# Performance work log

Measured on AMD Instinct MI355X. Metric: run time of the kernel, lower is better.

The kernel has to match this reference:

```python
import jax, jax.numpy as jnp
from jax import lax
import numpy as np

P = 9  # patch_size


def unfold9(img):
    # img: (C, H, W) -> (C, P*P, L) with L = (H//P)*(W//P), non-overlapping patches
    C, H, W = img.shape
    x = img.reshape(C, H // P, P, W // P, P)
    x = x.transpose(0, 2, 4, 1, 3).reshape(C, P * P, (H // P) * (W // P))
    return x


def fold9(blocks, H, W):
    # blocks: (C, P*P, L) -> (C, H, W), inverse of unfold9 (no overlaps)
    C = blocks.shape[0]
    x = blocks.reshape(C, P, P, H // P, W // P)
    return x.transpose(0, 3, 1, 4, 2).reshape(C, H, W)


def avgpool3d_k3s2p1(x):
    # AvgPool3d(kernel=3, stride=2, padding=1, count_include_pad=False) on (B,C,D,H,W)
    win = (1, 1, 3, 3, 3)
    strides = (1, 1, 2, 2, 2)
    pad = [(0, 0), (0, 0), (1, 1), (1, 1), (1, 1)]
    s = lax.reduce_window(x, 0.0, lax.add, win, strides, pad)
    cnt = lax.reduce_window(jnp.ones_like(x[:1, :1]), 0.0, lax.add, win, strides, pad)
    return s / cnt


def setup_inputs() -> dict:
    key = jax.random.key(0)
    k = jax.random.split(key, 7)
    in1, in2, out = 32, 64, 64
    x = jax.random.normal(k[0], (1, in1, 36, 72, 72), jnp.float32)
    y = jax.random.normal(k[1], (1, in2, 18, 36, 36), jnp.float32)
    z = jax.random.normal(k[2], (1, out, 36, 72, 72), jnp.float32)
    w_img = jax.random.normal(k[3], (out, in1), jnp.float32) * 0.05
    b_img = jax.random.normal(k[4], (out,), jnp.float32) * 0.01
    w_fea = jax.random.normal(k[5], (out, in2), jnp.float32) * 0.05
    b_fea = jax.random.normal(k[6], (out,), jnp.float32) * 0.01
    return {"x": x, "y": y, "z": z, "w_img": w_img, "b_img": b_img,
            "w_fea": w_fea, "b_fea": b_fea}


def reference(x, y, z, w_img, b_img, w_fea, b_fea):
    # 1x1x1 conv projections (pointwise channel mix)
    xq = jnp.einsum('bcdhw,oc->bodhw', x, w_img) + b_img[None, :, None, None, None]
    yk = jnp.einsum('bcdhw,oc->bodhw', y, w_fea) + b_fea[None, :, None, None, None]
    C = xq.shape[1]
    D1, HW1 = xq.shape[2], xq.shape[3] * xq.shape[4]
    D2, HW2 = yk.shape[2], yk.shape[3] * yk.shape[4]
    Ux = unfold9(xq.reshape(C, D1, HW1))          # (C, 81, L1)
    Uy = unfold9(yk.reshape(C, D2, HW2))          # (C, 81, L2)
    att = jnp.einsum('ckl,ckm->clm', Ux, Uy)      # (C, L1, L2) per-channel patch attn

    # --- Cross_head ---
    Dd, Hd, Wd = z.shape[2], z.shape[3], z.shape[4]
    dec = z.reshape(C, Dd, Hd * Wd)               # decoder_reshape
    xd = avgpool3d_k3s2p1(z)                      # (1, C, Dd', Hd', Wd')
    Dp, HWp = xd.shape[2], xd.shape[3] * xd.shape[4]
    Uxd = unfold9(xd.reshape(C, Dp, HWp))         # (C, 81, L2)
    # count_nonzero along L2 (non-differentiable, matches torch)
    nz = jnp.sum(att != 0, axis=-1).astype(att.dtype) + 1e-5  # (C, L1)
    corr_blocks = jnp.einsum('clm,ckm->ckl', att / nz[:, :, None], Uxd)  # (C, 81, L1)
    corr = fold9(corr_blocks, Dd, Hd * Wd)        # (C, Dd, Hd*Wd)
    act = jnp.where(corr > 0, corr, 0.2 * corr)   # LeakyReLU(0.2)
    out = act * dec + dec
    return out.reshape(z.shape)
```

## Files before the change

### kernel.cpp

```cpp
#include <hip/hip_runtime.h>
#include <hip/hip_bf16.h>

typedef __hip_bfloat16 bf16;
typedef float in_t;
typedef float out_t;
typedef __attribute__((ext_vector_type(8))) short short8;
typedef __attribute__((ext_vector_type(4))) float f32x4;

#define CH    64
#define CIN1  32
#define CIN2  64
#define S1    186624
#define W1    5184
#define S2    23328
#define W2    1296
#define LDSTR 1297
#define BSTR  104
#define XSTR  134
#define OSTR  136
#define YSTR  68
#define HWSTR 76
#define INV_NZ (1.0f/(288.0f + 1e-5f))

#define NB_PL 1152
#define NB_PX 1458
#define NB_PY 365

static __device__ __forceinline__ unsigned short f2bu(float f) {
    bf16 h = __float2bfloat16(f);
    unsigned short u;
    __builtin_memcpy(&u, &h, 2);
    return u;
}

__global__ __launch_bounds__(256) void k_stage1(
    const in_t* __restrict__ x, const in_t* __restrict__ wi, const in_t* __restrict__ bi,
    bf16* __restrict__ xq,
    const in_t* __restrict__ y, const in_t* __restrict__ wf, const in_t* __restrict__ bf,
    float* __restrict__ yk,
    const in_t* __restrict__ z, float* __restrict__ xd)
{
    __shared__ __align__(16) char smem[22528];
    int bid = blockIdx.x;
    int t   = threadIdx.x;

    if (bid < NB_PL) {
        float* dsum = reinterpret_cast<float*>(smem);
        int c = bid / 18, od = bid - (bid/18)*18;
        int dlo = od ? 2*od - 1 : 0;
        int nd  = od ? 3 : 2;
        const float4* zp = reinterpret_cast<const float4*>(z + ((size_t)c*36 + dlo)*W1);
        if (nd == 3) {
            for (int i = t; i < 1296; i += 256) {
                float4 a = zp[i], b = zp[1296 + i], e = zp[2592 + i];
                float4 s = { a.x+b.x+e.x, a.y+b.y+e.y, a.z+b.z+e.z, a.w+b.w+e.w };
                int r = i / 18, q = i - (i/18)*18;
                *reinterpret_cast<float4*>(&dsum[r*HWSTR + q*4]) = s;
            }
        } else {
            for (int i = t; i < 1296; i += 256) {
                float4 a = zp[i], b = zp[1296 + i];
                float4 s = { a.x+b.x, a.y+b.y, a.z+b.z, a.w+b.w };
                int r = i / 18, q = i - (i/18)*18;
                *reinterpret_cast<float4*>(&dsum[r*HWSTR + q*4]) = s;
            }
        }
        __syncthreads();
        float icd = (nd == 3) ? (1.f/3.f) : 0.5f;
        float* xdp = xd + (size_t)c*S2 + (size_t)od*W2;
        for (int idx = t; idx < 1296; idx += 256) {
            int oh = idx / 36, ow = idx - (idx/36)*36;
            int h0 = oh ? 2*oh-1 : 0, h1 = 2*oh+1;
            int w0 = ow ? 2*ow-1 : 0, w1 = 2*ow+1;
            float s = 0.f;
            for (int h = h0; h <= h1; ++h)
                for (int w = w0; w <= w1; ++w)
                    s += dsum[h*HWSTR + w];
            float ich = (h1 - h0) == 1 ? 0.5f : (1.f/3.f);
            float icw = (w1 - w0) == 1 ? 0.5f : (1.f/3.f);
            xdp[idx] = s * icd * ich * icw;
        }
    } else if (bid < NB_PL + NB_PX) {
        float*          xl = reinterpret_cast<float*>(smem);
        unsigned short* wl = reinterpret_cast<unsigned short*>(smem + CIN1*XSTR*4);
        int gs0 = (bid - NB_PL)*128;
        #pragma unroll
        for (int i = 0; i < 4; ++i) {
            int fi = t + i*256;
            int c  = fi >> 5, s4 = fi & 31;
            float4 v = *reinterpret_cast<const float4*>(&x[(size_t)c*S1 + gs0 + s4*4]);
            float* dst = &xl[c*XSTR + s4*4];
            *reinterpret_cast<float2*>(dst)     = (float2){v.x, v.y};
            *reinterpret_cast<float2*>(dst + 2) = (float2){v.z, v.w};
        }
        #pragma unroll
        for (int i = 0; i < 2; ++i) {
            int wj = t + i*256;
            int o  = wj >> 3, c4 = wj & 7;
            float4 v = *reinterpret_cast<const float4*>(&wi[o*CIN1 + c4*4]);
            ushort4 u = { f2bu(v.x), f2bu(v.y), f2bu(v.z), f2bu(v.w) };
            *reinterpret_cast<ushort4*>(&wl[o*CIN1 + c4*4]) = u;
        }
        int l = t & 63, wv = t >> 6;
        int lcol = l & 15, loct = l >> 4;
        float bly[4];
        #pragma unroll
        for (int og = 0; og < 4; ++og) bly[og] = bi[og*16 + lcol];
        __syncthreads();

        short8 wfr[4];
        #pragma unroll
        for (int og = 0; og < 4; ++og)
            wfr[og] = *reinterpret_cast<const short8*>(&wl[(og*16 + lcol)*CIN1 + loct*8]);

        ushort4 rr[2][4];
        #pragma unroll
        for (int mt = 0; mt < 2; ++mt) {
            int s_base = (wv*2 + mt)*16;
            union { short8 v; unsigned short u[8]; } af;
            #pragma unroll
            for (int j = 0; j < 8; ++j)
                af.u[j] = f2bu(xl[(loct*8 + j)*XSTR + s_base + lcol]);
            #pragma unroll
            for (int og = 0; og < 4; ++og) {
                f32x4 d = { bly[og], bly[og], bly[og], bly[og] };
                d = __builtin_amdgcn_mfma_f32_16x16x32_bf16(af.v, wfr[og], d, 0, 0, 0);
                rr[mt][og] = (ushort4){ f2bu(d[0]), f2bu(d[1]), f2bu(d[2]), f2bu(d[3]) };
            }
        }
        __syncthreads();
        unsigned short* ot = reinterpret_cast<unsigned short*>(smem);
        #pragma unroll
        for (int mt = 0; mt < 2; ++mt)
            #pragma unroll
            for (int og = 0; og < 4; ++og)
                *reinterpret_cast<ushort4*>(
                    &ot[(og*16 + lcol)*OSTR + wv*32 + mt*16 + loct*4]) = rr[mt][og];
        __syncthreads();
        #pragma unroll
        for (int j = 0; j < 4; ++j) {
            int row = wv*16 + j*4 + (l >> 4);
            int c8  = l & 15;
            uint4 v = *reinterpret_cast<const uint4*>(&ot[row*OSTR + c8*8]);
            *reinterpret_cast<uint4*>(
                (unsigned short*)xq + (size_t)row*S1 + gs0 + c8*8) = v;
        }
    } else {
        int pyb   = bid - NB_PL - NB_PX;
        int sblk0 = pyb*64;
        int wv = t >> 6, l = t & 63;
        int lcol = l & 15, loct = l >> 4;
        int tile = pyb*4 + wv;
        float* ot = reinterpret_cast<float*>(smem);
        bool act = (tile < 1458);
        f32x4 dv[4];
        if (act) {
            int s0 = tile*16;
            union { short8 v; unsigned short u[8]; } af[2];
            #pragma unroll
            for (int kk = 0; kk < 2; ++kk)
                #pragma unroll
                for (int j = 0; j < 8; ++j)
                    af[kk].u[j] = f2bu(y[(size_t)(kk*32 + loct*8 + j)*S2 + s0 + lcol]);
            #pragma unroll
            for (int og = 0; og < 4; ++og) {
                int o = og*16 + lcol;
                union { short8 v; unsigned short u[8]; } wfr[2];
                #pragma unroll
                for (int kk = 0; kk < 2; ++kk) {
                    float4 a  = *reinterpret_cast<const float4*>(&wf[o*CIN2 + kk*32 + loct*8]);
                    float4 bq = *reinterpret_cast<const float4*>(&wf[o*CIN2 + kk*32 + loct*8 + 4]);
                    wfr[kk].u[0]=f2bu(a.x);  wfr[kk].u[1]=f2bu(a.y);
                    wfr[kk].u[2]=f2bu(a.z);  wfr[kk].u[3]=f2bu(a.w);
                    wfr[kk].u[4]=f2bu(bq.x); wfr[kk].u[5]=f2bu(bq.y);
                    wfr[kk].u[6]=f2bu(bq.z); wfr[kk].u[7]=f2bu(bq.w);
                }
                float bo = bf[o];
                f32x4 d = { bo, bo, bo, bo };
                d = __builtin_amdgcn_mfma_f32_16x16x32_bf16(af[0].v, wfr[0].v, d, 0, 0, 0);
                d = __builtin_amdgcn_mfma_f32_16x16x32_bf16(af[1].v, wfr[1].v, d, 0, 0, 0);
                dv[og] = d;
            }
            #pragma unroll
            for (int og = 0; og < 4; ++og)
                *reinterpret_cast<float4*>(
                    &ot[(og*16 + lcol)*YSTR + wv*16 + loct*4]) =
                    (float4){ dv[og][0], dv[og][1], dv[og][2], dv[og][3] };
        }
        __syncthreads();
        #pragma unroll
        for (int j = 0; j < 4; ++j) {
            int row = wv*16 + j*4 + (l >> 4);
            int c4  = l & 15;
            int s   = sblk0 + c4*4;
            if (s < S2) {
                float4 v = *reinterpret_cast<const float4*>(&ot[row*YSTR + c4*4]);
                *reinterpret_cast<float4*>(&yk[(size_t)row*S2 + s]) = v;
            }
        }
    }
}

__global__ __launch_bounds__(256) void k_M(
    const float* __restrict__ xd, const float* __restrict__ yk, unsigned short* __restrict__ Mg)
{
    __shared__ float xl[3*LDSTR];
    __shared__ float yl[3*LDSTR];
    int b = blockIdx.x;
    int c = b / 9, r = b - c*9;
    int g = r / 3, h = r - g*3;
    int t = threadIdx.x;
    int t1 = t / 27, t2 = t - (t/27)*27;
    int offx[3];
    #pragma unroll
    for (int a = 0; a < 3; ++a) {
        int kl = t1*3 + a;
        offx[a] = (kl/9)*LDSTR + (kl - (kl/9)*9);
    }
    int offy = (t2/9)*LDSTR + (t2 - (t2/9)*9);
    float acc[3] = {};
    for (int ph2 = 0; ph2 < 2; ++ph2) {
        __syncthreads();
        for (int idx = t; idx < 3*W2; idx += 256) {
            int rr = idx / W2, col = idx - rr*W2;
            xl[rr*LDSTR + col] = xd[c*S2 + (ph2*9 + g*3 + rr)*W2 + col];
            yl[rr*LDSTR + col] = yk[c*S2 + (ph2*9 + h*3 + rr)*W2 + col];
        }
        __syncthreads();
        if (t < 243) {
            for (int m = 0; m < 144; ++m) {
                int cb = m*9;
                float yv = yl[cb + offy];
                #pragma unroll
                for (int a = 0; a < 3; ++a)
                    acc[a] += xl[cb + offx[a]] * yv;
            }
        }
    }
    if (t < 243) {
        #pragma unroll
        for (int a = 0; a < 3; ++a) {
            int k1 = g*27 + t1*3 + a;
            Mg[c*9216 + k1*96 + (h*27 + t2)] = f2bu(acc[a]);
        }
    }
    if (r == 0) {
        for (int idx = t; idx < 2655; idx += 256) {
            int row, col;
            if (idx < 1440) { int q = idx/96; row = 81 + q; col = idx - q*96; }
            else { int j = idx - 1440; int q = j/15; row = q; col = 81 + (j - q*15); }
            Mg[c*9216 + row*96 + col] = 0;
        }
    }
}

__global__ __launch_bounds__(256, 4) void k_corr(
    const unsigned short* __restrict__ Mg, const bf16* __restrict__ xq,
    const in_t* __restrict__ z, out_t* __restrict__ out)
{
    __shared__ __align__(16) unsigned short Pl[192*BSTR];
    int bid = blockIdx.x;
    int c   = bid / 12;
    int rem = bid - c*12;
    int ph  = rem / 3;
    int ck  = rem - ph*3;
    int colbase = ck*1728;
    int t = threadIdx.x;

    for (int idx = t; idx < 192*15; idx += 256) {
        int r = idx/15;
        Pl[r*BSTR + 81 + (idx - r*15)] = 0;
    }
    const unsigned short* xqu =
        (const unsigned short*)(xq + (size_t)c*S1 + (size_t)(ph*9)*W1 + colbase);
    for (int idx = t; idx < 3888; idx += 256) {
        int i2 = idx / 432, v4 = idx - i2*432;
        ushort4 vv = *reinterpret_cast<const ushort4*>(xqu + (size_t)i2*W1 + v4*4);
        int col = v4*4;
        unsigned short uu[4] = {vv.x, vv.y, vv.z, vv.w};
        #pragma unroll
        for (int j = 0; j < 4; ++j) {
            int cc = col + j;
            int p = cc/9, j2 = cc - p*9;
            Pl[p*BSTR + i2*9 + j2] = uu[j];
        }
    }
    __syncthreads();

    int wv = t >> 6, l = t & 63;
    int lrow = l & 15, lhi = l >> 4;

    short8 bfr[3][3];
    #pragma unroll
    for (int ntl = 0; ntl < 3; ++ntl) {
        int n = (wv*3 + ntl)*16 + lrow;
        #pragma unroll
        for (int kk = 0; kk < 3; ++kk)
            bfr[ntl][kk] = *reinterpret_cast<const short8*>(&Pl[n*BSTR + kk*32 + lhi*8]);
    }

    f32x4 acc[6][3];
    #pragma unroll
    for (int mt = 0; mt < 6; ++mt)
        #pragma unroll
        for (int ntl = 0; ntl < 3; ++ntl)
            acc[mt][ntl] = (f32x4){0.f,0.f,0.f,0.f};

    const unsigned short* Mc = Mg + c*9216;
    #pragma unroll
    for (int mt = 0; mt < 6; ++mt) {
        short8 afr[3];
        #pragma unroll
        for (int kk = 0; kk < 3; ++kk)
            afr[kk] = *reinterpret_cast<const short8*>(Mc + (mt*16 + lrow)*96 + kk*32 + lhi*8);
        #pragma unroll
        for (int ntl = 0; ntl < 3; ++ntl) {
            f32x4 d = acc[mt][ntl];
            #pragma unroll
            for (int kk = 0; kk < 3; ++kk)
                d = __builtin_amdgcn_mfma_f32_16x16x32_bf16(afr[kk], bfr[ntl][kk], d, 0, 0, 0);
            acc[mt][ntl] = d;
        }
    }
    __syncthreads();

    float* stage = reinterpret_cast<float*>(Pl);
    #pragma unroll
    for (int pass = 0; pass < 2; ++pass) {
        if ((wv >> 1) == pass) {
            #pragma unroll
            for (int mt = 0; mt < 6; ++mt)
                #pragma unroll
                for (int ntl = 0; ntl < 3; ++ntl) {
                    int n = (wv*3 + ntl)*16 + lrow - pass*96;
                    #pragma unroll
                    for (int r = 0; r < 4; ++r) {
                        int m = mt*16 + lhi*4 + r;
                        if (m <= 80) {
                            int i = m/9, j = m - 9*i;
                            stage[i*864 + n*9 + j] = acc[mt][ntl][r];
                        }
                    }
                }
        }
        __syncthreads();
        for (int idx = t; idx < 1944; idx += 256) {
            int i = idx/216, c4 = idx - i*216;
            float4 sv = *reinterpret_cast<const float4*>(&stage[i*864 + c4*4]);
            int ga = c*S1 + (ph*9 + i)*W1 + colbase + pass*864 + c4*4;
            float4 dv = *reinterpret_cast<const float4*>(&z[ga]);
            float4 ov;
            float cr;
            cr = sv.x*INV_NZ; ov.x = dv.x + (cr > 0.f ? cr : 0.2f*cr)*dv.x;
            cr = sv.y*INV_NZ; ov.y = dv.y + (cr > 0.f ? cr : 0.2f*cr)*dv.y;
            cr = sv.z*INV_NZ; ov.z = dv.z + (cr > 0.f ? cr : 0.2f*cr)*dv.z;
            cr = sv.w*INV_NZ; ov.w = dv.w + (cr > 0.f ? cr : 0.2f*cr)*dv.w;
            *reinterpret_cast<float4*>(&out[ga]) = ov;
        }
        __syncthreads();
    }
}

extern "C" void kernel_launch(void* const* d_in, const int* in_sizes, int n_in,
                              void* d_out, int out_size, void* d_ws, size_t ws_size,
                              hipStream_t stream)
{
    (void)in_sizes; (void)n_in; (void)out_size; (void)ws_size;
    const in_t* x     = (const in_t*)d_in[0];
    const in_t* y     = (const in_t*)d_in[1];
    const in_t* z     = (const in_t*)d_in[2];
    const in_t* w_img = (const in_t*)d_in[3];
    const in_t* b_img = (const in_t*)d_in[4];
    const in_t* w_fea = (const in_t*)d_in[5];
    const in_t* b_fea = (const in_t*)d_in[6];
    out_t* out = (out_t*)d_out;

    char* ws = (char*)d_ws;
    bf16*           xq = (bf16*)          (ws + 0);
    float*          yk = (float*)         (ws + 23887872);
    float*          xd = (float*)         (ws + 29859840);
    unsigned short* Mg = (unsigned short*)(ws + 35831808);

    hipLaunchKernelGGL(k_stage1, dim3(NB_PL + NB_PX + NB_PY), dim3(256), 0, stream,
                       x, w_img, b_img, xq, y, w_fea, b_fea, yk, z, xd);
    hipLaunchKernelGGL(k_M,      dim3(576), dim3(256), 0, stream, xd, yk, Mg);
    hipLaunchKernelGGL(k_corr,   dim3(768), dim3(256), 0, stream, Mg, xq, z, out);
}
```

Measured before the change: 82.08 us.

## Fuse three stage kernels into one persistent cooperative kernel with grid syncs

Merges the projection/pooling, M-computation and correlation kernels into a single cooperative launch. Each block loops over the virtual block indices of each stage, and grid-wide barriers separate the stages. This is meant to remove two kernel launch boundaries and their drain/ramp gaps. In exchange, shared memory is sized for the largest stage, the grid is capped by occupancy, grid.sync adds its own cost, and the launch-bounds hint now applies to all stages.

```diff
diff --git a/kernel.cpp b/kernel.cpp
--- a/kernel.cpp
+++ b/kernel.cpp
@@ -1,5 +1,8 @@
 #include <hip/hip_runtime.h>
 #include <hip/hip_bf16.h>
+#include <hip/hip_cooperative_groups.h>
+
+namespace cg = cooperative_groups;
 
 typedef __hip_bfloat16 bf16;
 typedef float in_t;
@@ -25,6 +28,9 @@
 #define NB_PL 1152
 #define NB_PX 1458
 #define NB_PY 365
+#define NBA   (NB_PL + NB_PX + NB_PY)
+#define NBB   576
+#define NBC   768
 
 static __device__ __forceinline__ unsigned short f2bu(float f) {
     bf16 h = __float2bfloat16(f);
@@ -33,20 +39,16 @@
     return u;
 }
 
-__global__ __launch_bounds__(256) void k_stage1(
+static __device__ void stageA_body(int vb, int t, char* smem,
     const in_t* __restrict__ x, const in_t* __restrict__ wi, const in_t* __restrict__ bi,
     bf16* __restrict__ xq,
-    const in_t* __restrict__ y, const in_t* __restrict__ wf, const in_t* __restrict__ bf,
+    const in_t* __restrict__ y, const in_t* __restrict__ wfe, const in_t* __restrict__ bfe,
     float* __restrict__ yk,
     const in_t* __restrict__ z, float* __restrict__ xd)
 {
-    __shared__ __align__(16) char smem[22528];
-    int bid = blockIdx.x;
-    int t   = threadIdx.x;
-
-    if (bid < NB_PL) {
+    if (vb < NB_PL) {
         float* dsum = reinterpret_cast<float*>(smem);
-        int c = bid / 18, od = bid - (bid/18)*18;
+        int c = vb / 18, od = vb - (vb/18)*18;
         int dlo = od ? 2*od - 1 : 0;
         int nd  = od ? 3 : 2;
         const float4* zp = reinterpret_cast<const float4*>(z + ((size_t)c*36 + dlo)*W1);
@@ -80,10 +82,10 @@
             float icw = (w1 - w0) == 1 ? 0.5f : (1.f/3.f);
             xdp[idx] = s * icd * ich * icw;
         }
-    } else if (bid < NB_PL + NB_PX) {
+    } else if (vb < NB_PL + NB_PX) {
         float*          xl = reinterpret_cast<float*>(smem);
         unsigned short* wl = reinterpret_cast<unsigned short*>(smem + CIN1*XSTR*4);
-        int gs0 = (bid - NB_PL)*128;
+        int gs0 = (vb - NB_PL)*128;
         #pragma unroll
         for (int i = 0; i < 4; ++i) {
             int fi = t + i*256;
@@ -146,15 +148,13 @@
                 (unsigned short*)xq + (size_t)row*S1 + gs0 + c8*8) = v;
         }
     } else {
-        int pyb   = bid - NB_PL - NB_PX;
+        int pyb   = vb - NB_PL - NB_PX;
         int sblk0 = pyb*64;
         int wv = t >> 6, l = t & 63;
         int lcol = l & 15, loct = l >> 4;
         int tile = pyb*4 + wv;
         float* ot = reinterpret_cast<float*>(smem);
-        bool act = (tile < 1458);
-        f32x4 dv[4];
-        if (act) {
+        if (tile < 1458) {
             int s0 = tile*16;
             union { short8 v; unsigned short u[8]; } af[2];
             #pragma unroll
@@ -168,24 +168,21 @@
                 union { short8 v; unsigned short u[8]; } wfr[2];
                 #pragma unroll
                 for (int kk = 0; kk < 2; ++kk) {
-                    float4 a  = *reinterpret_cast<const float4*>(&wf[o*CIN2 + kk*32 + loct*8]);
-                    float4 bq = *reinterpret_cast<const float4*>(&wf[o*CIN2 + kk*32 + loct*8 + 4]);
+                    float4 a  = *reinterpret_cast<const float4*>(&wfe[o*CIN2 + kk*32 + loct*8]);
+                    float4 bq = *reinterpret_cast<const float4*>(&wfe[o*CIN2 + kk*32 + loct*8 + 4]);
                     wfr[kk].u[0]=f2bu(a.x);  wfr[kk].u[1]=f2bu(a.y);
                     wfr[kk].u[2]=f2bu(a.z);  wfr[kk].u[3]=f2bu(a.w);
                     wfr[kk].u[4]=f2bu(bq.x); wfr[kk].u[5]=f2bu(bq.y);
                     wfr[kk].u[6]=f2bu(bq.z); wfr[kk].u[7]=f2bu(bq.w);
                 }
-                float bo = bf[o];
+                float bo = bfe[o];
                 f32x4 d = { bo, bo, bo, bo };
                 d = __builtin_amdgcn_mfma_f32_16x16x32_bf16(af[0].v, wfr[0].v, d, 0, 0, 0);
                 d = __builtin_amdgcn_mfma_f32_16x16x32_bf16(af[1].v, wfr[1].v, d, 0, 0, 0);
-                dv[og] = d;
-            }
-            #pragma unroll
-            for (int og = 0; og < 4; ++og)
                 *reinterpret_cast<float4*>(
                     &ot[(og*16 + lcol)*YSTR + wv*16 + loct*4]) =
-                    (float4){ dv[og][0], dv[og][1], dv[og][2], dv[og][3] };
+                    (float4){ d[0], d[1], d[2], d[3] };
+            }
         }
         __syncthreads();
         #pragma unroll
@@ -201,15 +198,14 @@
     }
 }
 
-__global__ __launch_bounds__(256) void k_M(
-    const float* __restrict__ xd, const float* __restrict__ yk, unsigned short* __restrict__ Mg)
+static __device__ void kM_body(int vb, int t, char* smem,
+    const float* __restrict__ xd, const float* __restrict__ yk,
+    unsigned short* __restrict__ Mg)
 {
-    __shared__ float xl[3*LDSTR];
-    __shared__ float yl[3*LDSTR];
-    int b = blockIdx.x;
-    int c = b / 9, r = b - c*9;
+    float* xl = reinterpret_cast<float*>(smem);
+    float* yl = xl + 3*LDSTR;
+    int c = vb / 9, r = vb - c*9;
     int g = r / 3, h = r - g*3;
-    int t = threadIdx.x;
     int t1 = t / 27, t2 = t - (t/27)*27;
     int offx[3];
     #pragma unroll
@@ -254,18 +250,16 @@
     }
 }
 
-__global__ __launch_bounds__(256, 4) void k_corr(
+static __device__ void kcorr_body(int vb, int t, char* smem,
     const unsigned short* __restrict__ Mg, const bf16* __restrict__ xq,
     const in_t* __restrict__ z, out_t* __restrict__ out)
 {
-    __shared__ __align__(16) unsigned short Pl[192*BSTR];
-    int bid = blockIdx.x;
-    int c   = bid / 12;
-    int rem = bid - c*12;
+    unsigned short* Pl = reinterpret_cast<unsigned short*>(smem);
+    int c   = vb / 12;
+    int rem = vb - c*12;
     int ph  = rem / 3;
     int ck  = rem - ph*3;
     int colbase = ck*1728;
-    int t = threadIdx.x;
 
     for (int idx = t; idx < 192*15; idx += 256) {
         int r = idx/15;
@@ -324,7 +318,7 @@
     }
     __syncthreads();
 
-    float* stage = reinterpret_cast<float*>(Pl);
+    float* stage = reinterpret_cast<float*>(smem);
     #pragma unroll
     for (int pass = 0; pass < 2; ++pass) {
         if ((wv >> 1) == pass) {
@@ -361,6 +355,34 @@
     }
 }
 
+__global__ __launch_bounds__(256, 4) void k_fused(
+    const in_t* __restrict__ x, const in_t* __restrict__ wi, const in_t* __restrict__ bi,
+    bf16* __restrict__ xq,
+    const in_t* __restrict__ y, const in_t* __restrict__ wfe, const in_t* __restrict__ bfe,
+    float* __restrict__ yk,
+    const in_t* __restrict__ z, float* __restrict__ xd,
+    unsigned short* __restrict__ Mg, out_t* __restrict__ out)
+{
+    __shared__ __align__(16) char smem[40960];
+    cg::grid_group grid = cg::this_grid();
+    int t = threadIdx.x;
+
+    for (int vb = blockIdx.x; vb < NBA; vb += gridDim.x) {
+        __syncthreads();
+        stageA_body(vb, t, smem, x, wi, bi, xq, y, wfe, bfe, yk, z, xd);
+    }
+    grid.sync();
+    for (int vb = blockIdx.x; vb < NBB; vb += gridDim.x) {
+        __syncthreads();
+        kM_body(vb, t, smem, xd, yk, Mg);
+    }
+    grid.sync();
+    for (int vb = blockIdx.x; vb < NBC; vb += gridDim.x) {
+        __syncthreads();
+        kcorr_body(vb, t, smem, Mg, xq, z, out);
+    }
+}
+
 extern "C" void kernel_launch(void* const* d_in, const int* in_sizes, int n_in,
                               void* d_out, int out_size, void* d_ws, size_t ws_size,
                               hipStream_t stream)
@@ -381,8 +403,16 @@
     float*          xd = (float*)         (ws + 29859840);
     unsigned short* Mg = (unsigned short*)(ws + 35831808);
 
-    hipLaunchKernelGGL(k_stage1, dim3(NB_PL + NB_PX + NB_PY), dim3(256), 0, stream,
-                       x, w_img, b_img, xq, y, w_fea, b_fea, yk, z, xd);
-    hipLaunchKernelGGL(k_M,      dim3(576), dim3(256), 0, stream, xd, yk, Mg);
-    hipLaunchKernelGGL(k_corr,   dim3(768), dim3(256), 0, stream, Mg, xq, z, out);
-}
+    int nb = 0;
+    if (hipOccupancyMaxActiveBlocksPerMultiprocessor(&nb, (const void*)k_fused, 256, 0)
+            != hipSuccess || nb < 1)
+        nb = 1;
+    int grid = nb * 256;
+    if (grid > 1024) grid = 1024;
+
+    void* args[] = { (void*)&x, (void*)&w_img, (void*)&b_img, (void*)&xq,
+                     (void*)&y, (void*)&w_fea, (void*)&b_fea, (void*)&yk,
+                     (void*)&z, (void*)&xd, (void*)&Mg, (void*)&out };
+    hipLaunchCooperativeKernel((const void*)k_fused, dim3(grid), dim3(256),
+                               args, 0, stream);
+}
```

Measured after the change: 302.2 us. 268% more time.

## Store pooled and projected intermediates as bf16 and split pooling blocks by half-height

Applied to the files above, without the earlier changes.

The intermediates yk (projected features) and xd (pooled decoder) are now written as bf16 instead of fp32 and expanded back to float when k_M loads them, halving their global traffic. The pooling blocks are also split into two halves along output height, doubling the pooling block count so each block reads and reduces fewer rows. This adds bf16 rounding ahead of the attention-matrix reduction, which may change accuracy, and the split reloads one overlapping input row per half.

```diff
diff --git a/kernel.cpp b/kernel.cpp
--- a/kernel.cpp
+++ b/kernel.cpp
@@ -22,7 +22,7 @@
 #define HWSTR 76
 #define INV_NZ (1.0f/(288.0f + 1e-5f))
 
-#define NB_PL 1152
+#define NB_PL 2304
 #define NB_PX 1458
 #define NB_PY 365
 
@@ -32,53 +32,66 @@
     __builtin_memcpy(&u, &h, 2);
     return u;
 }
+static __device__ __forceinline__ float bu2f(unsigned short u) {
+    unsigned int v = ((unsigned int)u) << 16;
+    float f;
+    __builtin_memcpy(&f, &v, 4);
+    return f;
+}
 
 __global__ __launch_bounds__(256) void k_stage1(
     const in_t* __restrict__ x, const in_t* __restrict__ wi, const in_t* __restrict__ bi,
     bf16* __restrict__ xq,
     const in_t* __restrict__ y, const in_t* __restrict__ wf, const in_t* __restrict__ bf,
-    float* __restrict__ yk,
-    const in_t* __restrict__ z, float* __restrict__ xd)
+    unsigned short* __restrict__ yk,
+    const in_t* __restrict__ z, unsigned short* __restrict__ xd)
 {
-    __shared__ __align__(16) char smem[22528];
+    __shared__ __align__(16) char smem[21504];
     int bid = blockIdx.x;
     int t   = threadIdx.x;
 
     if (bid < NB_PL) {
         float* dsum = reinterpret_cast<float*>(smem);
-        int c = bid / 18, od = bid - (bid/18)*18;
+        int c  = bid / 36;
+        int rr = bid - c*36;
+        int od = rr >> 1, half = rr & 1;
+        int hbase = half ? 35 : 0;
+        int nrows = half ? 37 : 36;
+        int oh0   = half ? 18 : 0;
         int dlo = od ? 2*od - 1 : 0;
         int nd  = od ? 3 : 2;
-        const float4* zp = reinterpret_cast<const float4*>(z + ((size_t)c*36 + dlo)*W1);
-        if (nd == 3) {
-            for (int i = t; i < 1296; i += 256) {
-                float4 a = zp[i], b = zp[1296 + i], e = zp[2592 + i];
-                float4 s = { a.x+b.x+e.x, a.y+b.y+e.y, a.z+b.z+e.z, a.w+b.w+e.w };
-                int r = i / 18, q = i - (i/18)*18;
-                *reinterpret_cast<float4*>(&dsum[r*HWSTR + q*4]) = s;
-            }
-        } else {
-            for (int i = t; i < 1296; i += 256) {
-                float4 a = zp[i], b = zp[1296 + i];
-                float4 s = { a.x+b.x, a.y+b.y, a.z+b.z, a.w+b.w };
-                int r = i / 18, q = i - (i/18)*18;
-                *reinterpret_cast<float4*>(&dsum[r*HWSTR + q*4]) = s;
-            }
+        const float* zb = z + ((size_t)c*36 + dlo)*W1;
+        for (int i = t; i < nrows*18; i += 256) {
+            int r = i / 18, q = i - (i/18)*18;
+            int off = (hbase + r)*18 + q;
+            const float4* p0 = reinterpret_cast<const float4*>(zb);
+            float4 a = p0[off], b = p0[1296 + off];
+            float4 s;
+            if (nd == 3) {
+                float4 e = p0[2592 + off];
+                s = (float4){ a.x+b.x+e.x, a.y+b.y+e.y, a.z+b.z+e.z, a.w+b.w+e.w };
+            } else {
+                s = (float4){ a.x+b.x, a.y+b.y, a.z+b.z, a.w+b.w };
+            }
+            *reinterpret_cast<float4*>(&dsum[r*HWSTR + q*4]) = s;
         }
         __syncthreads();
         float icd = (nd == 3) ? (1.f/3.f) : 0.5f;
-        float* xdp = xd + (size_t)c*S2 + (size_t)od*W2;
-        for (int idx = t; idx < 1296; idx += 256) {
-            int oh = idx / 36, ow = idx - (idx/36)*36;
+        unsigned short* xdp = xd + (size_t)c*S2 + (size_t)od*W2 + oh0*36;
+        for (int idx = t; idx < 648; idx += 256) {
+            int ohl = idx / 36, ow = idx - (idx/36)*36;
+            int oh = oh0 + ohl;
             int h0 = oh ? 2*oh-1 : 0, h1 = 2*oh+1;
             int w0 = ow ? 2*ow-1 : 0, w1 = 2*ow+1;
             float s = 0.f;
-            for (int h = h0; h <= h1; ++h)
+            for (int h = h0; h <= h1; ++h) {
+                int lr = h - hbase;
                 for (int w = w0; w <= w1; ++w)
-                    s += dsum[h*HWSTR + w];
+                    s += dsum[lr*HWSTR + w];
+            }
             float ich = (h1 - h0) == 1 ? 0.5f : (1.f/3.f);
             float icw = (w1 - w0) == 1 ? 0.5f : (1.f/3.f);
-            xdp[idx] = s * icd * ich * icw;
+            xdp[idx] = f2bu(s * icd * ich * icw);
         }
     } else if (bid < NB_PL + NB_PX) {
         float*          xl = reinterpret_cast<float*>(smem);
@@ -151,10 +164,8 @@
         int wv = t >> 6, l = t & 63;
         int lcol = l & 15, loct = l >> 4;
         int tile = pyb*4 + wv;
-        float* ot = reinterpret_cast<float*>(smem);
-        bool act = (tile < 1458);
-        f32x4 dv[4];
-        if (act) {
+        unsigned short* ot = reinterpret_cast<unsigned short*>(smem);
+        if (tile < 1458) {
             int s0 = tile*16;
             union { short8 v; unsigned short u[8]; } af[2];
             #pragma unroll
@@ -179,13 +190,9 @@
                 f32x4 d = { bo, bo, bo, bo };
                 d = __builtin_amdgcn_mfma_f32_16x16x32_bf16(af[0].v, wfr[0].v, d, 0, 0, 0);
                 d = __builtin_amdgcn_mfma_f32_16x16x32_bf16(af[1].v, wfr[1].v, d, 0, 0, 0);
-                dv[og] = d;
-            }
-            #pragma unroll
-            for (int og = 0; og < 4; ++og)
-                *reinterpret_cast<float4*>(
-                    &ot[(og*16 + lcol)*YSTR + wv*16 + loct*4]) =
-                    (float4){ dv[og][0], dv[og][1], dv[og][2], dv[og][3] };
+                ushort4 r4 = { f2bu(d[0]), f2bu(d[1]), f2bu(d[2]), f2bu(d[3]) };
+                *reinterpret_cast<ushort4*>(&ot[(og*16 + lcol)*YSTR + wv*16 + loct*4]) = r4;
+            }
         }
         __syncthreads();
         #pragma unroll
@@ -194,15 +201,16 @@
             int c4  = l & 15;
             int s   = sblk0 + c4*4;
             if (s < S2) {
-                float4 v = *reinterpret_cast<const float4*>(&ot[row*YSTR + c4*4]);
-                *reinterpret_cast<float4*>(&yk[(size_t)row*S2 + s]) = v;
+                ushort4 v = *reinterpret_cast<const ushort4*>(&ot[row*YSTR + c4*4]);
+                *reinterpret_cast<ushort4*>(&yk[(size_t)row*S2 + s]) = v;
             }
         }
     }
 }
 
 __global__ __launch_bounds__(256) void k_M(
-    const float* __restrict__ xd, const float* __restrict__ yk, unsigned short* __restrict__ Mg)
+    const unsigned short* __restrict__ xd, const unsigned short* __restrict__ yk,
+    unsigned short* __restrict__ Mg)
 {
     __shared__ float xl[3*LDSTR];
     __shared__ float yl[3*LDSTR];
@@ -223,8 +231,8 @@
         __syncthreads();
         for (int idx = t; idx < 3*W2; idx += 256) {
             int rr = idx / W2, col = idx - rr*W2;
-            xl[rr*LDSTR + col] = xd[c*S2 + (ph2*9 + g*3 + rr)*W2 + col];
-            yl[rr*LDSTR + col] = yk[c*S2 + (ph2*9 + h*3 + rr)*W2 + col];
+            xl[rr*LDSTR + col] = bu2f(xd[c*S2 + (ph2*9 + g*3 + rr)*W2 + col]);
+            yl[rr*LDSTR + col] = bu2f(yk[c*S2 + (ph2*9 + h*3 + rr)*W2 + col]);
         }
         __syncthreads();
         if (t < 243) {
@@ -377,9 +385,9 @@
 
     char* ws = (char*)d_ws;
     bf16*           xq = (bf16*)          (ws + 0);
-    float*          yk = (float*)         (ws + 23887872);
-    float*          xd = (float*)         (ws + 29859840);
-    unsigned short* Mg = (unsigned short*)(ws + 35831808);
+    unsigned short* yk = (unsigned short*)(ws + 23887872);
+    unsigned short* xd = (unsigned short*)(ws + 26873856);
+    unsigned short* Mg = (unsigned short*)(ws + 29859840);
 
     hipLaunchKernelGGL(k_stage1, dim3(NB_PL + NB_PX + NB_PY), dim3(256), 0, stream,
                        x, w_img, b_img, xq, y, w_fea, b_fea, yk, z, xd);
```

Measured after the change: 82.66 us. No clear change (+0.7%).
